# Performance work log

Hardware: AMD Instinct MI355X
Metric: run time of the kernel (lower is better)

## Reference

```python
import jax, jax.numpy as jnp
import numpy as np

N_NODES = 50000
N_EDGES = 800000
NUM_GRAPHS = 128
KS = 5           # kernel_size per pseudo dim
K = KS * KS      # 25 spline weight matrices per layer


def spline_coeff(pseudo):
    """Open linear (degree-1) B-spline basis for 2-D pseudo coords in [0,1].
    Returns dense per-edge coefficients over the K=25 kernel slots: [E, K]."""
    pos = pseudo * (KS - 1)                      # [E,2]
    lo = jnp.clip(jnp.floor(pos).astype(jnp.int32), 0, KS - 2)
    frac = pos - lo.astype(pseudo.dtype)         # [E,2]
    i0, i1 = lo, lo + 1
    w0, w1 = 1.0 - frac, frac
    # 2^dim = 4 corner combinations, flat index = d0 + KS*d1
    idx = jnp.stack([i0[:, 0] + KS * i0[:, 1],
                     i0[:, 0] + KS * i1[:, 1],
                     i1[:, 0] + KS * i0[:, 1],
                     i1[:, 0] + KS * i1[:, 1]], axis=1)            # [E,4]
    w = jnp.stack([w0[:, 0] * w0[:, 1], w0[:, 0] * w1[:, 1],
                   w1[:, 0] * w0[:, 1], w1[:, 0] * w1[:, 1]], axis=1)  # [E,4]
    E = pseudo.shape[0]
    coeff = jnp.zeros((E, K), pseudo.dtype).at[jnp.arange(E)[:, None], idx].add(w)
    return coeff


def spline_conv(x, coeff, src, dst, W, root, bias):
    """SplineConv: gather src feats, spline-weighted transform, scatter-mean to dst,
    plus root weight and bias. x:[N,in], coeff:[E,K], W:[K,in,out]."""
    n = x.shape[0]
    x_src = x[src]                                # [E,in] gather
    m = coeff[:, 0:1] * (x_src @ W[0])            # [E,out]
    for k in range(1, K):                         # fixed small loop over K kernels
        m = m + coeff[:, k:k + 1] * (x_src @ W[k])
    agg = jax.ops.segment_sum(m, dst, num_segments=n)
    cnt = jax.ops.segment_sum(jnp.ones((src.shape[0],), x.dtype), dst, num_segments=n)
    agg = agg / jnp.maximum(cnt, 1.0)[:, None]    # mean aggregation (PyG default)
    return agg + x @ root + bias


def setup_inputs() -> dict:
    key = jax.random.key(0)
    ks = jax.random.split(key, 16)
    s = 0.1  # small init scale for numerical stability
    return {
        "x": jax.random.normal(ks[0], (N_NODES, 1), jnp.float32),
        "position": jax.random.uniform(ks[1], (N_NODES, 2), jnp.float32),
        "pseudo": jax.random.uniform(ks[2], (N_EDGES, 2), jnp.float32),
        "edge_index": jax.random.randint(ks[3], (2, N_EDGES), 0, N_NODES, jnp.int32),
        "batch": jnp.sort(jax.random.randint(ks[4], (N_NODES,), 0, NUM_GRAPHS, jnp.int32)),
        "W1": s * jax.random.normal(ks[5], (K, 1, 32), jnp.float32),
        "root1": s * jax.random.normal(ks[6], (1, 32), jnp.float32),
        "b1": jnp.zeros((32,), jnp.float32),
        "W2": s * jax.random.normal(ks[7], (K, 32, 64), jnp.float32),
        "root2": s * jax.random.normal(ks[8], (32, 64), jnp.float32),
        "b2": jnp.zeros((64,), jnp.float32),
        "W3": s * jax.random.normal(ks[9], (K, 64, 64), jnp.float32),
        "root3": s * jax.random.normal(ks[10], (64, 64), jnp.float32),
        "b3": jnp.zeros((64,), jnp.float32),
        "fc_w": s * jax.random.normal(ks[11], (64, 10), jnp.float32),
        "fc_b": jnp.zeros((10,), jnp.float32),
    }


def reference(x, position, pseudo, edge_index, batch,
              W1, root1, b1, W2, root2, b2, W3, root3, b3, fc_w, fc_b):
    # `position` is accepted but unused, matching the original forward.
    src, dst = edge_index[0], edge_index[1]
    coeff = spline_coeff(pseudo)
    h = jax.nn.elu(spline_conv(x, coeff, src, dst, W1, root1, b1))
    h = jax.nn.elu(spline_conv(h, coeff, src, dst, W2, root2, b2))
    h = jax.nn.elu(spline_conv(h, coeff, src, dst, W3, root3, b3))
    # scatter_mean pooling over batch indices -> [NUM_GRAPHS, 64]
    pooled = jax.ops.segment_sum(h, batch, num_segments=NUM_GRAPHS)
    gcnt = jax.ops.segment_sum(jnp.ones((h.shape[0],), h.dtype), batch,
                               num_segments=NUM_GRAPHS)
    pooled = pooled / jnp.maximum(gcnt, 1.0)[:, None]
    # dropout is identity in eval mode
    logits = pooled @ fc_w + fc_b
    return jax.nn.log_softmax(logits, axis=1)
```

## Files before the change

kernel.cpp:

```cpp
#include <hip/hip_runtime.h>

#define NN 50000
#define NE 800000
#define NG 128
#define NB_SCAN 196

typedef unsigned int uint;
typedef unsigned short ushort;
typedef __attribute__((ext_vector_type(8))) short short8;
typedef __attribute__((ext_vector_type(4))) float f32x4;
typedef __attribute__((ext_vector_type(16))) float f32x16;

__device__ __forceinline__ float bf2f(ushort u){ union{uint i; float f;} v; v.i=(uint)u<<16; return v.f; }
__device__ __forceinline__ ushort f2bf(float f){ union{float f; uint i;} v; v.f=f; return (ushort)((v.i + 0x7FFFu + ((v.i>>16)&1u))>>16); }
__device__ __forceinline__ int iswz(int i){ return i ^ ((i>>4)&3); }

__global__ void zero_k(int* hist, float* pooled, int* gcnt){
    int i = blockIdx.x*blockDim.x + threadIdx.x;
    if (i < NN) hist[i] = 0;
    if (i < NG*64) pooled[i] = 0.f;
    if (i < NG) gcnt[i] = 0;
}

__global__ void hist_k(const int* __restrict__ ei, int* __restrict__ hist){
    int e = blockIdx.x*blockDim.x + threadIdx.x;
    if (e < NE) atomicAdd(&hist[ei[NE + e]], 1);
}

__global__ __launch_bounds__(256) void scan1(const int* __restrict__ hist, int* __restrict__ bsum){
    __shared__ int sm[256];
    int t = threadIdx.x, i = blockIdx.x*256 + t;
    sm[t] = (i < NN) ? hist[i] : 0;
    __syncthreads();
    for (int o = 128; o > 0; o >>= 1){ if (t < o) sm[t] += sm[t+o]; __syncthreads(); }
    if (t == 0) bsum[blockIdx.x] = sm[0];
}
__global__ __launch_bounds__(256) void scan2(const int* __restrict__ bsum, int* __restrict__ bpre){
    __shared__ int sm[256];
    int t = threadIdx.x;
    int v = (t < NB_SCAN) ? bsum[t] : 0;
    sm[t] = v; __syncthreads();
    int acc = v;
    for (int o = 1; o < 256; o <<= 1){
        int u = (t >= o) ? sm[t-o] : 0; __syncthreads();
        acc += u; sm[t] = acc; __syncthreads();
    }
    if (t < NB_SCAN) bpre[t] = acc - v;
}
__global__ __launch_bounds__(256) void scan3(const int* __restrict__ hist, const int* __restrict__ bpre,
                                             int* __restrict__ offs, int* __restrict__ cursor,
                                             float* __restrict__ invc){
    __shared__ int sm[256];
    int t = threadIdx.x, b = blockIdx.x, i = b*256 + t;
    int v = (i < NN) ? hist[i] : 0;
    sm[t] = v; __syncthreads();
    int acc = v;
    for (int o = 1; o < 256; o <<= 1){
        int u = (t >= o) ? sm[t-o] : 0; __syncthreads();
        acc += u; sm[t] = acc; __syncthreads();
    }
    int excl = acc - v + bpre[b];
    if (i < NN){ offs[i] = excl; cursor[i] = excl; invc[i] = 1.0f/(float)max(v,1); }
    if (i == NN-1) offs[NN] = NE;
}

__global__ void scatter_k(const int* __restrict__ ei, const float* __restrict__ pseudo,
                          int* __restrict__ cursor, uint4* __restrict__ payA, uint* __restrict__ payB){
    int e = blockIdx.x*blockDim.x + threadIdx.x;
    if (e >= NE) return;
    float2 ps = *(const float2*)(pseudo + 2*(size_t)e);
    float px = ps.x * 4.0f, py = ps.y * 4.0f;
    int lx = min(max((int)floorf(px), 0), 3);
    int ly = min(max((int)floorf(py), 0), 3);
    float fx = px - (float)lx, fy = py - (float)ly;
    float gx = 1.f - fx, gy = 1.f - fy;
    float w00 = gx*gy, w10 = fx*gy, w01 = gx*fy, w11 = fx*fy;
    ushort h00 = f2bf(w00), h10 = f2bf(w10), h01 = f2bf(w01), h11 = f2bf(w11);
    ushort L00 = f2bf(w00 - bf2f(h00)), L10 = f2bf(w10 - bf2f(h10));
    ushort L01 = f2bf(w01 - bf2f(h01)), L11 = f2bf(w11 - bf2f(h11));
    uint meta = (uint)ei[e] | ((uint)lx<<16) | ((uint)ly<<18);
    int pos = atomicAdd(&cursor[ei[NE + e]], 1);
    payA[pos] = make_uint4(meta, (uint)h00 | ((uint)h10<<16),
                                 (uint)h01 | ((uint)h11<<16),
                                 (uint)L00 | ((uint)L10<<16));
    payB[pos] = (uint)L01 | ((uint)L11<<16);
}

template<int IN>
__global__ void wprep_k(const float* __restrict__ W, const float* __restrict__ root, ushort* __restrict__ Bp){
    const int total = 26*IN*64;
    int tid = blockIdx.x*blockDim.x + threadIdx.x;
    if (tid >= total) return;
    int j    = tid & 7;
    int lane = (tid >> 3) & 63;
    int ctkt = tid >> 9;
    int ct   = ctkt & 3;
    int kt   = ctkt >> 2;
    int kk   = kt*32 + (lane>>4)*8 + j;
    int col  = ct*16 + (lane & 15);
    float v;
    if (kk < 25*IN){ int k = kk / IN; int i = kk % IN; v = W[((size_t)k*IN + i)*64 + col]; }
    else           { v = root[(size_t)(kk - 25*IN)*64 + col]; }
    Bp[tid] = f2bf(v);
}

__global__ __launch_bounds__(256) void reduce1_k(const float* __restrict__ x, const uint4* __restrict__ payA,
                                                 const uint* __restrict__ payB,
                                                 const int* __restrict__ offs, const float* __restrict__ invc,
                                                 const float* __restrict__ W1, const float* __restrict__ root1,
                                                 const float* __restrict__ b1, ushort* __restrict__ h1bf){
    __shared__ float w1s[25*32];
    for (int i = threadIdx.x; i < 25*32; i += 256) w1s[i] = W1[i];
    __syncthreads();
    int wid  = threadIdx.x >> 6;
    int lane = threadIdx.x & 63;
    int o    = lane & 31;
    int half = lane >> 5;
    int d    = blockIdx.x*4 + wid;
    int s = offs[d], e = offs[d+1];
    float acc = 0.f;
    for (int p = s; p < e; ++p){
        uint4 q0 = payA[p];
        uint lo23 = payB[p];
        uint meta = q0.x;
        int lx = (meta>>16)&3, ly = (meta>>18)&3;
        float wa, wb;
        if (half == 0){ wa = bf2f((ushort)q0.y) + bf2f((ushort)q0.w);
                        wb = bf2f((ushort)q0.z) + bf2f((ushort)lo23); }
        else          { wa = bf2f((ushort)(q0.y>>16)) + bf2f((ushort)(q0.w>>16));
                        wb = bf2f((ushort)(q0.z>>16)) + bf2f((ushort)(lo23>>16)); }
        float xs = x[meta & 0xFFFF];
        int ka = ly*5 + lx + half;
        acc += (wa*w1s[ka*32 + o] + wb*w1s[(ka+5)*32 + o]) * xs;
    }
    acc += __shfl_xor(acc, 32);
    if (half == 0){
        float val = acc*invc[d] + x[d]*root1[o] + b1[o];
        val = val > 0.f ? val : expm1f(val);
        h1bf[(size_t)d*32 + o] = f2bf(val);
    }
}

template<int IN, int MODE>
__global__ __launch_bounds__(512) void fused_r13(
        const ushort* __restrict__ hin, const uint4* __restrict__ payA, const uint* __restrict__ payB,
        const int* __restrict__ offs, const float* __restrict__ invc,
        const ushort* __restrict__ Bp, const float* __restrict__ bias,
        const int* __restrict__ batch, ushort* __restrict__ hout,
        float* __restrict__ pooled, int* __restrict__ gcnt)
{
    constexpr int NCT = IN/32;
    constexpr int KT  = 26*IN/32, KH = KT/2;
    __shared__ __align__(16) ushort Sb[KT*512];
    __shared__ __align__(16) uint4 eA[8][16];
    __shared__ uint eB[8][16];
    __shared__ float red[1024];
    __shared__ float outS[1024];

    const int tid = threadIdx.x, lane = tid & 63, w = tid >> 6;
    const int ln31 = lane & 31, kg2 = lane >> 5;
    const int d0 = blockIdx.x * 16;
    const int i0 = ln31 % 5, j0 = ln31 / 5;
    const bool rv = (ln31 < 25);

    for (int nn = 0; nn < 2; ++nn){
        const int node = w*2 + nn;
        const int d = d0 + node;
        int s = offs[d];
        int h = offs[d+1] - s;
        int steps = (h + 15) >> 4;

        f32x16 accH[NCT];
        #pragma unroll
        for (int ct = 0; ct < NCT; ++ct)
            #pragma unroll
            for (int q = 0; q < 16; ++q) accH[ct][q] = 0.f;

        uint4 vA = make_uint4(0u,0u,0u,0u); uint vB = 0u;
        {
            int rem = (h < 16) ? h : 16;
            if (lane < rem) vA = payA[(size_t)s + lane];
            int j2 = lane - 16;
            if (j2 >= 0 && j2 < rem) vB = payB[(size_t)s + j2];
        }
        for (int ks = 0; ks < steps; ++ks){
            if (lane < 16) eA[w][lane] = vA;
            else if (lane < 32) eB[w][lane-16] = vB;
            if (ks+1 < steps){
                int rem = h - (ks+1)*16; if (rem > 16) rem = 16;
                uint4 nA = make_uint4(0u,0u,0u,0u); uint nB = 0u;
                if (lane < rem) nA = payA[(size_t)(s + (ks+1)*16) + lane];
                int j2 = lane - 16;
                if (j2 >= 0 && j2 < rem) nB = payB[(size_t)(s + (ks+1)*16) + j2];
                vA = nA; vB = nB;
            }
            short8 ah, al;
            uint srcs[8];
            #pragma unroll
            for (int j = 0; j < 8; ++j){
                int es = kg2*8 + j;
                uint4 q0  = eA[w][es];
                uint lo23 = eB[w][es];
                uint meta = q0.x;
                int lx = (meta>>16)&3, ly = (meta>>18)&3;
                int dx = i0 - lx, dy = j0 - ly;
                bool ok = rv && ((uint)dx < 2u) && ((uint)dy < 2u);
                uint hiw = (dy == 1) ? q0.z : q0.y;
                uint low = (dy == 1) ? lo23 : q0.w;
                int sh = (dx & 1) << 4;
                ah[j] = ok ? (short)((hiw >> sh) & 0xFFFFu) : (short)0;
                al[j] = ok ? (short)((low >> sh) & 0xFFFFu) : (short)0;
                srcs[j] = meta & 0xFFFFu;
            }
            short8 bfv[NCT];
            #pragma unroll
            for (int j = 0; j < 8; ++j){
                const ushort* hb = hin + (size_t)srcs[j]*IN + ln31;
                #pragma unroll
                for (int ct = 0; ct < NCT; ++ct)
                    bfv[ct][j] = (short)hb[ct*32];
            }
            #pragma unroll
            for (int ct = 0; ct < NCT; ++ct){
                accH[ct] = __builtin_amdgcn_mfma_f32_32x32x16_bf16(ah, bfv[ct], accH[ct], 0, 0, 0);
                accH[ct] = __builtin_amdgcn_mfma_f32_32x32x16_bf16(al, bfv[ct], accH[ct], 0, 0, 0);
            }
        }

        {
            float ic = invc[d];
            int jd  = ln31 & 7;
            int l3  = ln31 >> 3;
            #pragma unroll
            for (int reg = 0; reg < 16; ++reg){
                int r = (reg & 3) + 8*(reg >> 2) + 4*kg2;
                if (r < 25){
                    #pragma unroll
                    for (int ct = 0; ct < NCT; ++ct){
                        int kt  = r*NCT + ct;
                        int kgt = (ct*4 + l3) & 3;
                        Sb[kt*512 + iswz(kgt*16 + node)*8 + jd] = f2bf(accH[ct][reg]*ic);
                    }
                }
            }
            if (IN == 64){
                int f = lane;
                Sb[(25*NCT + (f>>5))*512 + iswz(((f>>3)&3)*16 + node)*8 + (f&7)] = hin[(size_t)d*64 + f];
            } else if (lane < 32){
                int f = lane;
                Sb[25*512 + iswz(((f>>3)&3)*16 + node)*8 + (f&7)] = hin[(size_t)d*32 + f];
            }
        }
    }
    __syncthreads();

    {
        int ct = w & 3, kh = w >> 2;
        int c15 = lane & 15, kg = lane >> 4;
        int ig = iswz(lane);
        f32x4 a4 = {0.f,0.f,0.f,0.f};
        const ushort* bb = Bp + ct*512 + (size_t)lane*8;
        #pragma unroll
        for (int k = 0; k < KH; ++k){
            int kt = kh*KH + k;
            short8 a = *(const short8*)(Sb + kt*512 + ig*8);
            short8 b = *(const short8*)(bb + (size_t)kt*2048);
            a4 = __builtin_amdgcn_mfma_f32_16x16x32_bf16(a, b, a4, 0, 0, 0);
        }
        if (kh == 1){
            float* rr = red + (ct*64 + lane)*4;
            rr[0]=a4[0]; rr[1]=a4[1]; rr[2]=a4[2]; rr[3]=a4[3];
        }
        __syncthreads();
        if (kh == 0){
            const float* rr = red + (ct*64 + lane)*4;
            int col = ct*16 + c15;
            float bs = bias[col];
            #pragma unroll
            for (int jq = 0; jq < 4; ++jq){
                int r16 = kg*4 + jq;
                float v = a4[jq] + rr[jq] + bs;
                v = v > 0.f ? v : expm1f(v);
                if (MODE == 0) ((ushort*)outS)[r16*64 + col] = f2bf(v);
                else           outS[r16*64 + col] = v;
            }
        }
    }
    __syncthreads();

    if (MODE == 0){
        uint* dst = (uint*)(hout + (size_t)d0*64);
        const uint* srcp = (const uint*)outS;
        dst[tid] = srcp[tid];
    } else {
        if (w == 0){
            int c = lane;
            float run = 0.f; int gprev = batch[d0];
            for (int r = 0; r < 16; ++r){
                int g = batch[d0 + r];
                if (g != gprev){ atomicAdd(&pooled[gprev*64 + c], run); run = 0.f; gprev = g; }
                run += outS[r*64 + c];
            }
            atomicAdd(&pooled[gprev*64 + c], run);
        } else if (w == 1 && lane == 0){
            int cnt = 0; int gprev = batch[d0];
            for (int r = 0; r < 16; ++r){
                int g = batch[d0 + r];
                if (g != gprev){ atomicAdd(&gcnt[gprev], cnt); cnt = 0; gprev = g; }
                cnt++;
            }
            atomicAdd(&gcnt[gprev], cnt);
        }
    }
}

__global__ __launch_bounds__(128) void head_k(const float* __restrict__ pooled, const int* __restrict__ gcnt,
                                              const float* __restrict__ fcw, const float* __restrict__ fcb,
                                              float* __restrict__ out){
    int g = threadIdx.x;
    if (g >= NG) return;
    float inv = 1.0f / fmaxf((float)gcnt[g], 1.0f);
    float logits[10];
    #pragma unroll
    for (int c = 0; c < 10; ++c) logits[c] = fcb[c];
    for (int o = 0; o < 64; ++o){
        float m = pooled[g*64 + o] * inv;
        #pragma unroll
        for (int c = 0; c < 10; ++c) logits[c] += m * fcw[o*10 + c];
    }
    float mx = logits[0];
    #pragma unroll
    for (int c = 1; c < 10; ++c) mx = fmaxf(mx, logits[c]);
    float ssum = 0.f;
    #pragma unroll
    for (int c = 0; c < 10; ++c) ssum += expf(logits[c] - mx);
    float lse = logf(ssum) + mx;
    #pragma unroll
    for (int c = 0; c < 10; ++c) out[g*10 + c] = logits[c] - lse;
}

extern "C" void kernel_launch(void* const* d_in, const int* in_sizes, int n_in,
                              void* d_out, int out_size, void* d_ws, size_t ws_size,
                              hipStream_t stream) {
    const float* x      = (const float*)d_in[0];
    const float* pseudo = (const float*)d_in[2];
    const int*   ei     = (const int*)  d_in[3];
    const int*   batch  = (const int*)  d_in[4];
    const float* W1     = (const float*)d_in[5];
    const float* root1  = (const float*)d_in[6];
    const float* b1     = (const float*)d_in[7];
    const float* W2     = (const float*)d_in[8];
    const float* root2  = (const float*)d_in[9];
    const float* b2     = (const float*)d_in[10];
    const float* W3     = (const float*)d_in[11];
    const float* root3  = (const float*)d_in[12];
    const float* b3     = (const float*)d_in[13];
    const float* fcw    = (const float*)d_in[14];
    const float* fcb    = (const float*)d_in[15];
    float* out = (float*)d_out;

    char* ws = (char*)d_ws;
    size_t off = 0;
    auto alloc = [&](size_t bytes)->char*{ char* p = ws + off; off += (bytes + 255) / 256 * 256; return p; };
    uint4*  payA   = (uint4*) alloc((size_t)NE*16);
    uint*   payB   = (uint*)  alloc((size_t)NE*4);
    ushort* h1bf   = (ushort*)alloc((size_t)NN*32*2);
    ushort* h2bf   = (ushort*)alloc((size_t)NN*64*2);
    int*    hist   = (int*)   alloc((size_t)NN*4);
    int*    offs   = (int*)   alloc((size_t)(NN+1)*4);
    int*    cursor = (int*)   alloc((size_t)NN*4);
    float*  invc   = (float*) alloc((size_t)NN*4);
    int*    bsum   = (int*)   alloc((size_t)NB_SCAN*4);
    int*    bpre   = (int*)   alloc((size_t)NB_SCAN*4);
    ushort* Bp2    = (ushort*)alloc((size_t)26*2048*2);
    ushort* Bp3    = (ushort*)alloc((size_t)52*2048*2);
    float*  pooled = (float*) alloc((size_t)NG*64*4);
    int*    gcnt   = (int*)   alloc((size_t)NG*4);
    (void)ws_size; (void)in_sizes; (void)n_in; (void)out_size;

    zero_k   <<<NB_SCAN, 256, 0, stream>>>(hist, pooled, gcnt);
    hist_k   <<<(NE+255)/256, 256, 0, stream>>>(ei, hist);
    scan1    <<<NB_SCAN, 256, 0, stream>>>(hist, bsum);
    scan2    <<<1, 256, 0, stream>>>(bsum, bpre);
    scan3    <<<NB_SCAN, 256, 0, stream>>>(hist, bpre, offs, cursor, invc);
    scatter_k<<<(NE+255)/256, 256, 0, stream>>>(ei, pseudo, cursor, payA, payB);
    wprep_k<32><<<(26*32*64 + 255)/256, 256, 0, stream>>>(W2, root2, Bp2);
    wprep_k<64><<<(26*64*64 + 255)/256, 256, 0, stream>>>(W3, root3, Bp3);
    reduce1_k<<<NN/4, 256, 0, stream>>>(x, payA, payB, offs, invc, W1, root1, b1, h1bf);
    fused_r13<32,0><<<NN/16, 512, 0, stream>>>(h1bf, payA, payB, offs, invc, Bp2, b2, batch, h2bf, pooled, gcnt);
    fused_r13<64,1><<<NN/16, 512, 0, stream>>>(h2bf, payA, payB, offs, invc, Bp3, b3, batch, h2bf, pooled, gcnt);
    head_k   <<<1, 128, 0, stream>>>(pooled, gcnt, fcw, fcb, out);
}
```

Before: 314.5 us.

## Specialize layer-3 fused kernel: 8 nodes per block, two-phase K staging, paired loads

Splits the templated fused kernel into a 32-wide version and a dedicated 64-wide layer-3 kernel. The 64-wide kernel handles 8 nodes per block (one per wave) instead of 16, and stages the 52 K-tiles through half-size shared memory in two phases separated by barriers. It also gathers two adjacent bf16 features per 32-bit load instead of two separate 16-bit loads. The aim is to lower shared-memory and register use so more blocks fit per CU, and to cut gather instructions. In exchange the weight GEMM runs in smaller M tiles with half of each 16-row MFMA idle, and the block needs extra barriers.

Result: slower. 346.1 us (+10.1%).

```diff
diff --git a/kernel.cpp b/kernel.cpp
--- a/kernel.cpp
+++ b/kernel.cpp
@@ -141,16 +141,15 @@
     }
 }
 
-template<int IN, int MODE>
-__global__ __launch_bounds__(512) void fused_r13(
+template<int MODE>
+__global__ __launch_bounds__(512) void fused32(
         const ushort* __restrict__ hin, const uint4* __restrict__ payA, const uint* __restrict__ payB,
         const int* __restrict__ offs, const float* __restrict__ invc,
         const ushort* __restrict__ Bp, const float* __restrict__ bias,
         const int* __restrict__ batch, ushort* __restrict__ hout,
         float* __restrict__ pooled, int* __restrict__ gcnt)
 {
-    constexpr int NCT = IN/32;
-    constexpr int KT  = 26*IN/32, KH = KT/2;
+    constexpr int KT = 26, KH = 13;
     __shared__ __align__(16) ushort Sb[KT*512];
     __shared__ __align__(16) uint4 eA[8][16];
     __shared__ uint eB[8][16];
@@ -170,11 +169,9 @@
         int h = offs[d+1] - s;
         int steps = (h + 15) >> 4;
 
-        f32x16 accH[NCT];
+        f32x16 accH;
         #pragma unroll
-        for (int ct = 0; ct < NCT; ++ct)
-            #pragma unroll
-            for (int q = 0; q < 16; ++q) accH[ct][q] = 0.f;
+        for (int q = 0; q < 16; ++q) accH[q] = 0.f;
 
         uint4 vA = make_uint4(0u,0u,0u,0u); uint vB = 0u;
         {
@@ -212,19 +209,12 @@
                 al[j] = ok ? (short)((low >> sh) & 0xFFFFu) : (short)0;
                 srcs[j] = meta & 0xFFFFu;
             }
-            short8 bfv[NCT];
+            short8 bfv;
             #pragma unroll
-            for (int j = 0; j < 8; ++j){
-                const ushort* hb = hin + (size_t)srcs[j]*IN + ln31;
-                #pragma unroll
-                for (int ct = 0; ct < NCT; ++ct)
-                    bfv[ct][j] = (short)hb[ct*32];
-            }
-            #pragma unroll
-            for (int ct = 0; ct < NCT; ++ct){
-                accH[ct] = __builtin_amdgcn_mfma_f32_32x32x16_bf16(ah, bfv[ct], accH[ct], 0, 0, 0);
-                accH[ct] = __builtin_amdgcn_mfma_f32_32x32x16_bf16(al, bfv[ct], accH[ct], 0, 0, 0);
-            }
+            for (int j = 0; j < 8; ++j)
+                bfv[j] = (short)hin[(size_t)srcs[j]*32 + ln31];
+            accH = __builtin_amdgcn_mfma_f32_32x32x16_bf16(ah, bfv, accH, 0, 0, 0);
+            accH = __builtin_amdgcn_mfma_f32_32x32x16_bf16(al, bfv, accH, 0, 0, 0);
         }
 
         {
@@ -234,22 +224,11 @@
             #pragma unroll
             for (int reg = 0; reg < 16; ++reg){
                 int r = (reg & 3) + 8*(reg >> 2) + 4*kg2;
-                if (r < 25){
-                    #pragma unroll
-                    for (int ct = 0; ct < NCT; ++ct){
-                        int kt  = r*NCT + ct;
-                        int kgt = (ct*4 + l3) & 3;
-                        Sb[kt*512 + iswz(kgt*16 + node)*8 + jd] = f2bf(accH[ct][reg]*ic);
-                    }
-                }
-            }
-            if (IN == 64){
-                int f = lane;
-                Sb[(25*NCT + (f>>5))*512 + iswz(((f>>3)&3)*16 + node)*8 + (f&7)] = hin[(size_t)d*64 + f];
-            } else if (lane < 32){
-                int f = lane;
-                Sb[25*512 + iswz(((f>>3)&3)*16 + node)*8 + (f&7)] = hin[(size_t)d*32 + f];
-            }
+                if (r < 25)
+                    Sb[r*512 + iswz(l3*16 + node)*8 + jd] = f2bf(accH[reg]*ic);
+            }
+            if (lane < 32)
+                Sb[25*512 + iswz(((lane>>3)&3)*16 + node)*8 + (lane&7)] = hin[(size_t)d*32 + lane];
         }
     }
     __syncthreads();
@@ -290,8 +269,7 @@
 
     if (MODE == 0){
         uint* dst = (uint*)(hout + (size_t)d0*64);
-        const uint* srcp = (const uint*)outS;
-        dst[tid] = srcp[tid];
+        dst[tid] = ((const uint*)outS)[tid];
     } else {
         if (w == 0){
             int c = lane;
@@ -307,6 +285,171 @@
             for (int r = 0; r < 16; ++r){
                 int g = batch[d0 + r];
                 if (g != gprev){ atomicAdd(&gcnt[gprev], cnt); cnt = 0; gprev = g; }
+                cnt++;
+            }
+            atomicAdd(&gcnt[gprev], cnt);
+        }
+    }
+}
+
+template<int MODE>
+__global__ __launch_bounds__(512) void fused64(
+        const ushort* __restrict__ hin, const uint4* __restrict__ payA, const uint* __restrict__ payB,
+        const int* __restrict__ offs, const float* __restrict__ invc,
+        const ushort* __restrict__ Bp, const float* __restrict__ bias,
+        const int* __restrict__ batch, ushort* __restrict__ hout,
+        float* __restrict__ pooled, int* __restrict__ gcnt)
+{
+    __shared__ __align__(16) ushort Sb[26*512];
+    __shared__ __align__(16) uint4 eA[8][16];
+    __shared__ uint eB[8][16];
+    __shared__ float red[1024];
+    __shared__ float outS[512];
+
+    const int tid = threadIdx.x, lane = tid & 63, w = tid >> 6;
+    const int ln31 = lane & 31, kg2 = lane >> 5;
+    const int d0 = blockIdx.x * 8;
+    const int d  = d0 + w;
+    const int i0 = ln31 % 5, j0 = ln31 / 5;
+    const bool rv = (ln31 < 25);
+
+    int s = offs[d];
+    int h = offs[d+1] - s;
+    int steps = (h + 15) >> 4;
+
+    f32x16 acc0, acc1;
+    #pragma unroll
+    for (int q = 0; q < 16; ++q){ acc0[q] = 0.f; acc1[q] = 0.f; }
+
+    {
+        uint4 vA = make_uint4(0u,0u,0u,0u); uint vB = 0u;
+        {
+            int rem = (h < 16) ? h : 16;
+            if (lane < rem) vA = payA[(size_t)s + lane];
+            int j2 = lane - 16;
+            if (j2 >= 0 && j2 < rem) vB = payB[(size_t)s + j2];
+        }
+        for (int ks = 0; ks < steps; ++ks){
+            if (lane < 16) eA[w][lane] = vA;
+            else if (lane < 32) eB[w][lane-16] = vB;
+            if (ks+1 < steps){
+                int rem = h - (ks+1)*16; if (rem > 16) rem = 16;
+                uint4 nA = make_uint4(0u,0u,0u,0u); uint nB = 0u;
+                if (lane < rem) nA = payA[(size_t)(s + (ks+1)*16) + lane];
+                int j2 = lane - 16;
+                if (j2 >= 0 && j2 < rem) nB = payB[(size_t)(s + (ks+1)*16) + j2];
+                vA = nA; vB = nB;
+            }
+            short8 ah, al;
+            uint hx[8];
+            #pragma unroll
+            for (int j = 0; j < 8; ++j){
+                int es = kg2*8 + j;
+                uint4 q0  = eA[w][es];
+                uint lo23 = eB[w][es];
+                uint meta = q0.x;
+                int lx = (meta>>16)&3, ly = (meta>>18)&3;
+                int dx = i0 - lx, dy = j0 - ly;
+                bool ok = rv && ((uint)dx < 2u) && ((uint)dy < 2u);
+                uint hiw = (dy == 1) ? q0.z : q0.y;
+                uint low = (dy == 1) ? lo23 : q0.w;
+                int sh = (dx & 1) << 4;
+                ah[j] = ok ? (short)((hiw >> sh) & 0xFFFFu) : (short)0;
+                al[j] = ok ? (short)((low >> sh) & 0xFFFFu) : (short)0;
+                hx[j] = *(const uint*)(hin + (size_t)(meta & 0xFFFFu)*64 + 2*ln31);
+            }
+            short8 b0, b1;
+            #pragma unroll
+            for (int j = 0; j < 8; ++j){
+                b0[j] = (short)(ushort)hx[j];
+                b1[j] = (short)(ushort)(hx[j] >> 16);
+            }
+            acc0 = __builtin_amdgcn_mfma_f32_32x32x16_bf16(ah, b0, acc0, 0, 0, 0);
+            acc0 = __builtin_amdgcn_mfma_f32_32x32x16_bf16(al, b0, acc0, 0, 0, 0);
+            acc1 = __builtin_amdgcn_mfma_f32_32x32x16_bf16(ah, b1, acc1, 0, 0, 0);
+            acc1 = __builtin_amdgcn_mfma_f32_32x32x16_bf16(al, b1, acc1, 0, 0, 0);
+        }
+    }
+
+    float ic = invc[d];
+    int ct = w & 3, g = w >> 2;
+    int c15 = lane & 15;
+    int ig = iswz(lane);
+    f32x4 a4 = {0.f,0.f,0.f,0.f};
+    const ushort* bb = Bp + ct*512 + (size_t)lane*8;
+
+    #pragma unroll
+    for (int P = 0; P < 2; ++P){
+        #pragma unroll
+        for (int reg = 0; reg < 16; ++reg){
+            int r = (reg & 3) + 8*(reg >> 2) + 4*kg2;
+            int rl = r - P*13;
+            if (rl >= 0 && rl < 13 && r < 25){
+                int off0 = 2*ln31;
+                int ktl0 = rl*2 + (off0>>5);
+                int kgp  = (off0>>3)&3;
+                int jd0  = off0&7;
+                int gsl  = iswz(kgp*16 + w)*8;
+                Sb[ktl0*512 + gsl + jd0]     = f2bf(acc0[reg]*ic);
+                Sb[ktl0*512 + gsl + jd0 + 1] = f2bf(acc1[reg]*ic);
+            }
+        }
+        if (P == 1){
+            int f = lane;
+            Sb[(24 + (f>>5))*512 + iswz(((f>>3)&3)*16 + w)*8 + (f&7)] = hin[(size_t)d*64 + f];
+        }
+        __syncthreads();
+        #pragma unroll
+        for (int k = 0; k < 13; ++k){
+            int ktl = g*13 + k;
+            int ktg = P*26 + ktl;
+            short8 a = *(const short8*)(Sb + ktl*512 + ig*8);
+            short8 b = *(const short8*)(bb + (size_t)ktg*2048);
+            a4 = __builtin_amdgcn_mfma_f32_16x16x32_bf16(a, b, a4, 0, 0, 0);
+        }
+        __syncthreads();
+    }
+
+    if (g == 1) *(f32x4*)&red[(ct*64 + lane)*4] = a4;
+    __syncthreads();
+    if (g == 0){
+        f32x4 rr = *(const f32x4*)&red[(ct*64 + lane)*4];
+        int kg = lane >> 4;
+        int col = ct*16 + c15;
+        float bs = bias[col];
+        #pragma unroll
+        for (int jq = 0; jq < 4; ++jq){
+            int r8 = kg*4 + jq;
+            if (r8 < 8){
+                float v = a4[jq] + rr[jq] + bs;
+                v = v > 0.f ? v : expm1f(v);
+                if (MODE == 0) ((ushort*)outS)[r8*64 + col] = f2bf(v);
+                else           outS[r8*64 + col] = v;
+            }
+        }
+    }
+    __syncthreads();
+
+    if (MODE == 0){
+        if (tid < 256){
+            uint* dst = (uint*)(hout + (size_t)d0*64);
+            dst[tid] = ((const uint*)outS)[tid];
+        }
+    } else {
+        if (w == 0){
+            int c = lane;
+            float run = 0.f; int gprev = batch[d0];
+            for (int r = 0; r < 8; ++r){
+                int gb = batch[d0 + r];
+                if (gb != gprev){ atomicAdd(&pooled[gprev*64 + c], run); run = 0.f; gprev = gb; }
+                run += outS[r*64 + c];
+            }
+            atomicAdd(&pooled[gprev*64 + c], run);
+        } else if (w == 1 && lane == 0){
+            int cnt = 0; int gprev = batch[d0];
+            for (int r = 0; r < 8; ++r){
+                int gb = batch[d0 + r];
+                if (gb != gprev){ atomicAdd(&gcnt[gprev], cnt); cnt = 0; gprev = gb; }
                 cnt++;
             }
             atomicAdd(&gcnt[gprev], cnt);
@@ -387,7 +530,7 @@
     wprep_k<32><<<(26*32*64 + 255)/256, 256, 0, stream>>>(W2, root2, Bp2);
     wprep_k<64><<<(26*64*64 + 255)/256, 256, 0, stream>>>(W3, root3, Bp3);
     reduce1_k<<<NN/4, 256, 0, stream>>>(x, payA, payB, offs, invc, W1, root1, b1, h1bf);
-    fused_r13<32,0><<<NN/16, 512, 0, stream>>>(h1bf, payA, payB, offs, invc, Bp2, b2, batch, h2bf, pooled, gcnt);
-    fused_r13<64,1><<<NN/16, 512, 0, stream>>>(h2bf, payA, payB, offs, invc, Bp3, b3, batch, h2bf, pooled, gcnt);
+    fused32<0><<<NN/16, 512, 0, stream>>>(h1bf, payA, payB, offs, invc, Bp2, b2, batch, h2bf, pooled, gcnt);
+    fused64<1><<<NN/8,  512, 0, stream>>>(h2bf, payA, payB, offs, invc, Bp3, b3, batch, h2bf, pooled, gcnt);
     head_k   <<<1, 128, 0, stream>>>(pooled, gcnt, fcw, fcb, out);
 }
```
